# Kernel tuning notes

Measured on AMD Instinct MI355X. Metric: run time of the kernel, lower is better.

## Reference

```python
import jax, jax.numpy as jnp
import numpy as np

DIM_IN = 1024
DIM_OUT = 1024
BATCH = 4
SEQ = 2048


def setup_inputs() -> dict:
    key = jax.random.key(0)
    kx, kq, kk, kv = jax.random.split(key, 4)
    scale = 1.0 / np.sqrt(DIM_IN)
    x = jax.random.normal(kx, (BATCH, SEQ, DIM_IN), dtype=jnp.float32)
    # Weights stored as [dim_in, dim_out] (transpose of torch Linear's [out, in]);
    # y = x @ W is equivalent math to torch's x @ W_t.T
    Wq = jax.random.normal(kq, (DIM_IN, DIM_OUT), dtype=jnp.float32) * scale
    Wk = jax.random.normal(kk, (DIM_IN, DIM_OUT), dtype=jnp.float32) * scale
    Wv = jax.random.normal(kv, (DIM_IN, DIM_OUT), dtype=jnp.float32) * scale
    return {"x": x, "Wq": Wq, "Wk": Wk, "Wv": Wv}


def reference(x, Wq, Wk, Wv):
    # x: [b, s, d_in]; single-head causal self-attention (dropout=0 -> identity)
    q = jnp.einsum("bsd,de->bse", x, Wq)
    k = jnp.einsum("bsd,de->bse", x, Wk)
    v = jnp.einsum("bsd,de->bse", x, Wv)
    dim_k = k.shape[-1]
    scores = jnp.einsum("bqe,bke->bqk", q, k) / jnp.sqrt(jnp.float32(dim_k))
    s = x.shape[1]
    causal = jnp.tril(jnp.ones((s, s), dtype=bool))  # True = keep
    scores = jnp.where(causal[None, :, :], scores, -jnp.inf)
    weights = jax.nn.softmax(scores, axis=-1)
    context = jnp.einsum("bqk,bke->bqe", weights, v)
    return context
```

## Files before the change

### kernel.cpp

```cpp
#include <hip/hip_runtime.h>
#include <cstdint>
#include <cstddef>

typedef unsigned short u16;
typedef __bf16 bf16x8 __attribute__((ext_vector_type(8)));
typedef float f32x4 __attribute__((ext_vector_type(4)));

__device__ inline u16 f2b(float f) {
    uint32_t u = __builtin_bit_cast(uint32_t, f);
    u += 0x7FFFu + ((u >> 16) & 1u);
    return (u16)(u >> 16);
}

__device__ inline void gl2lds16(const u16* g, u16* l) {
    __builtin_amdgcn_global_load_lds(
        (const __attribute__((address_space(1))) void*)g,
        (__attribute__((address_space(3))) void*)l, 16, 0, 0);
}

__global__ void prep_kernel(const float* __restrict__ x, u16* __restrict__ xb,
                            const float* __restrict__ Wq,
                            const float* __restrict__ Wk,
                            const float* __restrict__ Wv,
                            u16* __restrict__ QKWT, u16* __restrict__ WvT,
                            float* __restrict__ out, float* __restrict__ l) {
    __shared__ u16 t[32][33];
    const int bid = blockIdx.x;
    if (bid < 8192) {
        size_t i = ((size_t)bid * 256 + threadIdx.x) * 4;
        float4 v = *(const float4*)(x + i);
        uint2 pack;
        pack.x = (uint32_t)f2b(v.x) | ((uint32_t)f2b(v.y) << 16);
        pack.y = (uint32_t)f2b(v.z) | ((uint32_t)f2b(v.w) << 16);
        *(uint2*)(xb + i) = pack;
        *(float4*)(out + i) = make_float4(0.f, 0.f, 0.f, 0.f);
        return;
    }
    if (bid >= 11264) {
        size_t i = ((size_t)(bid - 11264) * 256 + threadIdx.x) * 4;
        *(float4*)(l + i) = make_float4(0.f, 0.f, 0.f, 0.f);
        return;
    }
    const int tb = bid - 8192;
    const int z = tb >> 10;
    const int rem = tb & 1023;
    const int by = (rem >> 5) * 32;
    const int bx = (rem & 31) * 32;
    const float* W = (z == 0) ? Wq : ((z == 1) ? Wk : Wv);
    u16* dst = (z == 0) ? QKWT : ((z == 1) ? QKWT + 1024 * 1024 : WvT);
    const float scale = (z == 0) ? 0.03125f : 1.0f;
    const int tx = threadIdx.x & 31, ty = threadIdx.x >> 5;
    #pragma unroll
    for (int r = 0; r < 32; r += 8)
        t[ty + r][tx] = f2b(W[(size_t)(by + ty + r) * 1024 + bx + tx] * scale);
    __syncthreads();
    #pragma unroll
    for (int r = 0; r < 32; r += 8)
        dst[(size_t)(bx + ty + r) * 1024 + (by + tx)] = t[tx][ty + r];
}

template<int EPI>
__device__ __forceinline__ void gemm_body(
    u16* __restrict__ smem,
    const u16* __restrict__ A, int lda,
    const u16* __restrict__ B, int ldb,
    char* __restrict__ Cb, int ldc,
    int m0, int n0, int Kloc, float* __restrict__ lrow, bool split = false) {
    constexpr int BK = 32;
    const int tid = threadIdx.x;
    const int lane = tid & 63, wave = tid >> 6;
    const int wm = wave >> 1, wn = wave & 1;
    const int fl = lane & 15, fh = lane >> 4;

    const int q0 = wave * 2;
    const int srow = lane >> 2, skoff = (lane & 3) * 8;
    const u16* ApL0 = A + (size_t)(m0 + q0 * 16 + srow) * lda + skoff;
    const u16* ApL1 = ApL0 + (size_t)16 * lda;
    const u16* BpL0 = B + (size_t)(n0 + q0 * 16 + srow) * ldb + skoff;
    const u16* BpL1 = BpL0 + (size_t)16 * ldb;

    u16* const Ab[2] = { smem, smem + 4096 };
    u16* const Bb[2] = { smem + 8192, smem + 12288 };

    auto issue = [&](int buf, int k0) {
        gl2lds16(ApL0 + k0, Ab[buf] + q0 * 512);
        gl2lds16(ApL1 + k0, Ab[buf] + q0 * 512 + 512);
        gl2lds16(BpL0 + k0, Bb[buf] + q0 * 512);
        gl2lds16(BpL1 + k0, Bb[buf] + q0 * 512 + 512);
    };

    const f32x4 vzero = {0.f, 0.f, 0.f, 0.f};
    f32x4 acc[4][4];
    #pragma unroll
    for (int i = 0; i < 4; ++i)
        #pragma unroll
        for (int j = 0; j < 4; ++j) acc[i][j] = vzero;

    issue(0, 0);
    int buf = 0;
    for (int k0 = 0; k0 < Kloc; k0 += BK, buf ^= 1) {
        __syncthreads();
        if (k0 + BK < Kloc) issue(buf ^ 1, k0 + BK);
        bf16x8 af[4], bfr[4];
        #pragma unroll
        for (int t = 0; t < 4; ++t) {
            af[t]  = *(const bf16x8*)&Ab[buf][(wm * 64 + t * 16 + fl) * BK + fh * 8];
            bfr[t] = *(const bf16x8*)&Bb[buf][(wn * 64 + t * 16 + fl) * BK + fh * 8];
        }
        #pragma unroll
        for (int mt = 0; mt < 4; ++mt)
            #pragma unroll
            for (int nt = 0; nt < 4; ++nt)
                acc[mt][nt] = __builtin_amdgcn_mfma_f32_16x16x32_bf16(
                    af[mt], bfr[nt], acc[mt][nt], 0, 0, 0);
    }

    if (EPI == 0) {
        u16* Cp = (u16*)Cb;
        #pragma unroll
        for (int mt = 0; mt < 4; ++mt)
            #pragma unroll
            for (int nt = 0; nt < 4; ++nt)
                #pragma unroll
                for (int r = 0; r < 4; ++r) {
                    int row = m0 + wm * 64 + mt * 16 + fh * 4 + r;
                    int col = n0 + wn * 64 + nt * 16 + fl;
                    Cp[(size_t)row * ldc + col] = f2b(acc[mt][nt][r]);
                }
    } else if (EPI == 2) {
        u16* Cp = (u16*)Cb;
        #pragma unroll
        for (int mt = 0; mt < 4; ++mt)
            #pragma unroll
            for (int r = 0; r < 4; ++r) {
                int row = m0 + wm * 64 + mt * 16 + fh * 4 + r;
                float part = 0.f;
                #pragma unroll
                for (int nt = 0; nt < 4; ++nt) {
                    int col = n0 + wn * 64 + nt * 16 + fl;
                    float p = (col <= row) ? __expf(acc[mt][nt][r]) : 0.f;
                    part += p;
                    Cp[(size_t)row * ldc + col] = f2b(p);
                }
                #pragma unroll
                for (int off = 1; off < 16; off <<= 1)
                    part += __shfl_xor(part, off, 64);
                if (fl == 0) atomicAdd(lrow + row, part);
            }
    } else {
        float* Cp = (float*)Cb;
        #pragma unroll
        for (int mt = 0; mt < 4; ++mt)
            #pragma unroll
            for (int r = 0; r < 4; ++r) {
                int row = m0 + wm * 64 + mt * 16 + fh * 4 + r;
                float inv = 1.0f / lrow[row];
                #pragma unroll
                for (int nt = 0; nt < 4; ++nt) {
                    int col = n0 + wn * 64 + nt * 16 + fl;
                    float v = acc[mt][nt][r] * inv;
                    if (split) atomicAdd(&Cp[(size_t)row * ldc + col], v);
                    else       Cp[(size_t)row * ldc + col] = v;
                }
            }
    }
}

__global__ __launch_bounds__(256)
void proj_kernel(const u16* __restrict__ xb, const u16* __restrict__ QKWT,
                 const u16* __restrict__ WvT, u16* __restrict__ QK,
                 u16* __restrict__ Vt) {
    __shared__ __align__(16) u16 smem[16384];
    int bid = blockIdx.x;
    if (bid < 1024) {
        int jt = bid & 15, it = bid >> 4;
        gemm_body<0>(smem, xb, 1024, QKWT, 1024, (char*)QK, 2048,
                     it * 128, jt * 128, 1024, nullptr);
    } else {
        int b = bid - 1024;
        int jt = b & 63, it = b >> 6;
        gemm_body<0>(smem, WvT, 1024, xb, 1024, (char*)Vt, 8192,
                     it * 128, jt * 128, 1024, nullptr);
    }
}

__global__ __launch_bounds__(256)
void scores_kernel(const u16* __restrict__ QK, u16* __restrict__ P,
                   float* __restrict__ l) {
    __shared__ __align__(16) u16 smem[16384];
    const int t = blockIdx.x, z = blockIdx.y;
    int it = (int)((sqrtf(8.0f * t + 1.0f) - 1.0f) * 0.5f);
    while ((it + 1) * (it + 2) / 2 <= t) ++it;
    while (it * (it + 1) / 2 > t) --it;
    const int jt = t - it * (it + 1) / 2;
    const u16* Qz = QK + (size_t)z * 2048 * 2048;
    const u16* Kz = Qz + 1024;
    u16* Pz = P + (size_t)z * 2048 * 2048;
    gemm_body<2>(smem, Qz, 2048, Kz, 2048, (char*)Pz, 2048,
                 it * 128, jt * 128, 1024, l + (size_t)z * 2048);
}

__global__ __launch_bounds__(256)
void out_kernel(const u16* __restrict__ P, const u16* __restrict__ Vt,
                float* __restrict__ out, float* __restrict__ l) {
    __shared__ __align__(16) u16 smem[16384];
    const int jt = blockIdx.x & 7, z = blockIdx.x >> 3;
    int c = blockIdx.y, it = 15;
    for (int i = 15; i >= 0; --i) {
        int n = (i >> 2) + 1;
        if (c < n) { it = i; break; }
        c -= n;
    }
    const int Ktot = (it + 1) * 128;
    const int k0 = c * 512;
    const int kloc = min(512, Ktot - k0);
    const bool split = (Ktot > 512);
    gemm_body<3>(smem, P + (size_t)z * 2048 * 2048 + k0, 2048,
                 Vt + (size_t)z * 2048 + k0, 8192,
                 (char*)(out + (size_t)z * 2048 * 1024), 1024,
                 it * 128, jt * 128, kloc, l + (size_t)z * 2048, split);
}

extern "C" void kernel_launch(void* const* d_in, const int* in_sizes, int n_in,
                              void* d_out, int out_size, void* d_ws, size_t ws_size,
                              hipStream_t stream) {
    (void)in_sizes; (void)n_in; (void)out_size; (void)ws_size;
    const float* x  = (const float*)d_in[0];
    const float* Wq = (const float*)d_in[1];
    const float* Wk = (const float*)d_in[2];
    const float* Wv = (const float*)d_in[3];
    float* out = (float*)d_out;

    const size_t MB = 1u << 20;
    char* ws = (char*)d_ws;
    u16* xb   = (u16*)(ws);
    u16* QKWT = (u16*)(ws + 16 * MB);
    u16* WvT  = (u16*)(ws + 20 * MB);
    u16* QK   = (u16*)(ws + 22 * MB);
    u16* Vt   = (u16*)(ws + 54 * MB);
    u16* P    = (u16*)(ws + 70 * MB);
    float* l  = (float*)(ws + 102 * MB);

    prep_kernel<<<8192 + 3072 + 8, 256, 0, stream>>>(x, xb, Wq, Wk, Wv, QKWT, WvT, out, l);
    proj_kernel<<<1536, 256, 0, stream>>>(xb, QKWT, WvT, QK, Vt);
    scores_kernel<<<dim3(136, 4), 256, 0, stream>>>(QK, P, l);
    out_kernel<<<dim3(32, 40), 256, 0, stream>>>(P, Vt, out, l);
}
```

Before: 289.7 us.

## Co-schedule V projection with scores GEMM and drop split-K atomics in output

Moves the V projection GEMM out of the projection kernel and into the same launch as the causal scores GEMM, so the QK projection runs alone and V-projection blocks fill the GPU alongside the triangular scores work. The output GEMM no longer splits K with atomicAdd. Each block now covers the full causal K range and stores plainly, and the zeroing of the output buffer in the prep kernel is removed. This saves the output memset and the atomic traffic, but leaves fewer, unevenly sized output blocks (512), with the largest ones scheduled first.

Result: faster. 258.0 us (-10.9%).

```diff
diff --git a/kernel.cpp b/kernel.cpp
--- a/kernel.cpp
+++ b/kernel.cpp
@@ -23,7 +23,7 @@
                             const float* __restrict__ Wk,
                             const float* __restrict__ Wv,
                             u16* __restrict__ QKWT, u16* __restrict__ WvT,
-                            float* __restrict__ out, float* __restrict__ l) {
+                            float* __restrict__ l) {
     __shared__ u16 t[32][33];
     const int bid = blockIdx.x;
     if (bid < 8192) {
@@ -33,7 +33,6 @@
         pack.x = (uint32_t)f2b(v.x) | ((uint32_t)f2b(v.y) << 16);
         pack.y = (uint32_t)f2b(v.z) | ((uint32_t)f2b(v.w) << 16);
         *(uint2*)(xb + i) = pack;
-        *(float4*)(out + i) = make_float4(0.f, 0.f, 0.f, 0.f);
         return;
     }
     if (bid >= 11264) {
@@ -65,7 +64,7 @@
     const u16* __restrict__ A, int lda,
     const u16* __restrict__ B, int ldb,
     char* __restrict__ Cb, int ldc,
-    int m0, int n0, int Kloc, float* __restrict__ lrow, bool split = false) {
+    int m0, int n0, int Kloc, float* __restrict__ lrow) {
     constexpr int BK = 32;
     const int tid = threadIdx.x;
     const int lane = tid & 63, wave = tid >> 6;
@@ -158,46 +157,45 @@
                 #pragma unroll
                 for (int nt = 0; nt < 4; ++nt) {
                     int col = n0 + wn * 64 + nt * 16 + fl;
-                    float v = acc[mt][nt][r] * inv;
-                    if (split) atomicAdd(&Cp[(size_t)row * ldc + col], v);
-                    else       Cp[(size_t)row * ldc + col] = v;
+                    Cp[(size_t)row * ldc + col] = acc[mt][nt][r] * inv;
                 }
             }
     }
 }
 
 __global__ __launch_bounds__(256)
-void proj_kernel(const u16* __restrict__ xb, const u16* __restrict__ QKWT,
-                 const u16* __restrict__ WvT, u16* __restrict__ QK,
-                 u16* __restrict__ Vt) {
+void projqk_kernel(const u16* __restrict__ xb, const u16* __restrict__ QKWT,
+                   u16* __restrict__ QK) {
     __shared__ __align__(16) u16 smem[16384];
-    int bid = blockIdx.x;
-    if (bid < 1024) {
-        int jt = bid & 15, it = bid >> 4;
-        gemm_body<0>(smem, xb, 1024, QKWT, 1024, (char*)QK, 2048,
-                     it * 128, jt * 128, 1024, nullptr);
+    const int jt = blockIdx.x & 15, it = blockIdx.x >> 4;
+    gemm_body<0>(smem, xb, 1024, QKWT, 1024, (char*)QK, 2048,
+                 it * 128, jt * 128, 1024, nullptr);
+}
+
+__global__ __launch_bounds__(256)
+void mid_kernel(const u16* __restrict__ QK, u16* __restrict__ P,
+                float* __restrict__ l,
+                const u16* __restrict__ WvT, const u16* __restrict__ xb,
+                u16* __restrict__ Vt) {
+    __shared__ __align__(16) u16 smem[16384];
+    const int bid = blockIdx.x;
+    if (bid < 544) {
+        const int z = bid / 136, t = bid - z * 136;
+        int it = (int)((sqrtf(8.0f * t + 1.0f) - 1.0f) * 0.5f);
+        while ((it + 1) * (it + 2) / 2 <= t) ++it;
+        while (it * (it + 1) / 2 > t) --it;
+        const int jt = t - it * (it + 1) / 2;
+        const u16* Qz = QK + (size_t)z * 2048 * 2048;
+        const u16* Kz = Qz + 1024;
+        u16* Pz = P + (size_t)z * 2048 * 2048;
+        gemm_body<2>(smem, Qz, 2048, Kz, 2048, (char*)Pz, 2048,
+                     it * 128, jt * 128, 1024, l + (size_t)z * 2048);
     } else {
-        int b = bid - 1024;
-        int jt = b & 63, it = b >> 6;
+        const int b = bid - 544;
+        const int jt = b & 63, it = b >> 6;
         gemm_body<0>(smem, WvT, 1024, xb, 1024, (char*)Vt, 8192,
                      it * 128, jt * 128, 1024, nullptr);
     }
-}
-
-__global__ __launch_bounds__(256)
-void scores_kernel(const u16* __restrict__ QK, u16* __restrict__ P,
-                   float* __restrict__ l) {
-    __shared__ __align__(16) u16 smem[16384];
-    const int t = blockIdx.x, z = blockIdx.y;
-    int it = (int)((sqrtf(8.0f * t + 1.0f) - 1.0f) * 0.5f);
-    while ((it + 1) * (it + 2) / 2 <= t) ++it;
-    while (it * (it + 1) / 2 > t) --it;
-    const int jt = t - it * (it + 1) / 2;
-    const u16* Qz = QK + (size_t)z * 2048 * 2048;
-    const u16* Kz = Qz + 1024;
-    u16* Pz = P + (size_t)z * 2048 * 2048;
-    gemm_body<2>(smem, Qz, 2048, Kz, 2048, (char*)Pz, 2048,
-                 it * 128, jt * 128, 1024, l + (size_t)z * 2048);
 }
 
 __global__ __launch_bounds__(256)
@@ -205,20 +203,11 @@
                 float* __restrict__ out, float* __restrict__ l) {
     __shared__ __align__(16) u16 smem[16384];
     const int jt = blockIdx.x & 7, z = blockIdx.x >> 3;
-    int c = blockIdx.y, it = 15;
-    for (int i = 15; i >= 0; --i) {
-        int n = (i >> 2) + 1;
-        if (c < n) { it = i; break; }
-        c -= n;
-    }
-    const int Ktot = (it + 1) * 128;
-    const int k0 = c * 512;
-    const int kloc = min(512, Ktot - k0);
-    const bool split = (Ktot > 512);
-    gemm_body<3>(smem, P + (size_t)z * 2048 * 2048 + k0, 2048,
-                 Vt + (size_t)z * 2048 + k0, 8192,
+    const int it = 15 - (int)blockIdx.y;
+    gemm_body<3>(smem, P + (size_t)z * 2048 * 2048, 2048,
+                 Vt + (size_t)z * 2048, 8192,
                  (char*)(out + (size_t)z * 2048 * 1024), 1024,
-                 it * 128, jt * 128, kloc, l + (size_t)z * 2048, split);
+                 it * 128, jt * 128, (it + 1) * 128, l + (size_t)z * 2048);
 }
 
 extern "C" void kernel_launch(void* const* d_in, const int* in_sizes, int n_in,
@@ -241,8 +230,8 @@
     u16* P    = (u16*)(ws + 70 * MB);
     float* l  = (float*)(ws + 102 * MB);
 
-    prep_kernel<<<8192 + 3072 + 8, 256, 0, stream>>>(x, xb, Wq, Wk, Wv, QKWT, WvT, out, l);
-    proj_kernel<<<1536, 256, 0, stream>>>(xb, QKWT, WvT, QK, Vt);
-    scores_kernel<<<dim3(136, 4), 256, 0, stream>>>(QK, P, l);
-    out_kernel<<<dim3(32, 40), 256, 0, stream>>>(P, Vt, out, l);
-}
+    prep_kernel<<<8192 + 3072 + 8, 256, 0, stream>>>(x, xb, Wq, Wk, Wv, QKWT, WvT, l);
+    projqk_kernel<<<1024, 256, 0, stream>>>(xb, QKWT, QK);
+    mid_kernel<<<1056, 256, 0, stream>>>(QK, P, l, WvT, xb, Vt);
+    out_kernel<<<dim3(32, 16), 256, 0, stream>>>(P, Vt, out, l);
+}
```
